# Optimization experiments

Measured on AMD Instinct MI355X. Metric: run time of the kernel, lower is better.

## Reference

```python
import jax, jax.numpy as jnp
import numpy as np

N = 100000      # n_nodes
D = 64          # d_model
E = 1_600_000   # n_edges
L = 3           # n_layers


def setup_inputs() -> dict:
    key = jax.random.key(0)
    ks = jax.random.split(key, 2 + 2 * L)
    x = jax.random.normal(ks[0], (N, D), dtype=jnp.float32)
    edge_index = jax.random.randint(ks[1], (2, E), 0, N, dtype=jnp.int32)
    inp = {"x": x, "edge_index": edge_index}
    scale = 1.0 / np.sqrt(D)
    for i in range(L):
        # GCNConv weight (glorot-ish init) and zero bias
        inp[f"W{i}"] = jax.random.uniform(ks[2 + 2 * i], (D, D), jnp.float32, -scale, scale)
        inp[f"b{i}"] = jnp.zeros((D,), jnp.float32)
    return inp


def gcn_conv(x, W, b, src, dst, num_nodes):
    # PyG GCNConv: h = x @ W, then D^{-1/2}(A+I)D^{-1/2} aggregation, then + b
    h = x @ W  # [N, D]
    ones = jnp.ones(dst.shape, dtype=h.dtype)
    deg = jax.ops.segment_sum(ones, dst, num_segments=num_nodes)  # [N]
    deg_inv_sqrt = jnp.where(deg > 0, jax.lax.rsqrt(jnp.maximum(deg, 1.0)), 0.0)
    norm = deg_inv_sqrt[src] * deg_inv_sqrt[dst]  # [E+N]
    msg = h[src] * norm[:, None]                  # gather + scale  [E+N, D]
    out = jax.ops.segment_sum(msg, dst, num_segments=num_nodes)  # scatter-add [N, D]
    return out + b


def reference(x, edge_index, W0, b0, W1, b1, W2, b2):
    num_nodes = x.shape[0]
    loop = jnp.arange(num_nodes, dtype=edge_index.dtype)
    src = jnp.concatenate([edge_index[0], loop])  # add self-loops
    dst = jnp.concatenate([edge_index[1], loop])
    h = x
    for W, b in ((W0, b0), (W1, b1), (W2, b2)):
        h = gcn_conv(h, W, b, src, dst, num_nodes)
        # F.dropout(training=self.training) is identity in eval mode
    return h
```

## Files before the change

kernel.cpp:

```cpp
#include <hip/hip_runtime.h>
#include <hip/hip_bf16.h>

#define D 64
#define RSHIFT 9
#define BNODES 512
#define MAXB 256
#define BCAP 10240
#define SCAP 14336
#define FH 72

typedef unsigned short ushort_t;
typedef unsigned int uint_t;
typedef short short8 __attribute__((ext_vector_type(8)));
typedef float floatx4 __attribute__((ext_vector_type(4)));

__device__ inline uint_t pk_bf16(float x, float y) {
    uint_t ux = __float_as_uint(x); ux = ux + 0x7fffu + ((ux >> 16) & 1u);
    uint_t uy = __float_as_uint(y); uy = uy + 0x7fffu + ((uy >> 16) & 1u);
    return (ux >> 16) | (uy & 0xffff0000u);
}
__device__ inline ushort_t rnd_bf16(float x) {
    uint_t u = __float_as_uint(x); u = u + 0x7fffu + ((u >> 16) & 1u);
    return (ushort_t)(u >> 16);
}

__global__ __launch_bounds__(256) void k_bucket(const int* __restrict__ src,
                                                const int* __restrict__ dst,
                                                int* __restrict__ bcur,
                                                int* __restrict__ ebuf,
                                                int E, int nb) {
    __shared__ int lcnt[MAXB];
    __shared__ int lbase[MAXB];
    int t = threadIdx.x;
    lcnt[t] = 0;
    __syncthreads();
    int base = blockIdx.x * 2048 + t * 8;
    int sv[8], dv[8], sl[8];
    if (base + 7 < E) {
        int4 a0 = *(const int4*)(src + base);
        int4 a1 = *(const int4*)(src + base + 4);
        int4 b0 = *(const int4*)(dst + base);
        int4 b1 = *(const int4*)(dst + base + 4);
        sv[0]=a0.x; sv[1]=a0.y; sv[2]=a0.z; sv[3]=a0.w;
        sv[4]=a1.x; sv[5]=a1.y; sv[6]=a1.z; sv[7]=a1.w;
        dv[0]=b0.x; dv[1]=b0.y; dv[2]=b0.z; dv[3]=b0.w;
        dv[4]=b1.x; dv[5]=b1.y; dv[6]=b1.z; dv[7]=b1.w;
    } else {
        #pragma unroll
        for (int j = 0; j < 8; ++j) {
            dv[j] = (base + j < E) ? dst[base + j] : -1;
            sv[j] = (base + j < E) ? src[base + j] : 0;
        }
    }
    #pragma unroll
    for (int j = 0; j < 8; ++j) {
        if (dv[j] >= 0) {
            int b = dv[j] >> RSHIFT;
            sl[j] = atomicAdd(&lcnt[b], 1);
        }
    }
    __syncthreads();
    if (t < nb) { int c = lcnt[t]; if (c) lbase[t] = atomicAdd(&bcur[t], c); }
    __syncthreads();
    #pragma unroll
    for (int j = 0; j < 8; ++j) {
        if (dv[j] >= 0) {
            int b = dv[j] >> RSHIFT;
            int slot = lbase[b] + sl[j];
            if (slot < BCAP)
                ebuf[(size_t)b * BCAP + slot] = (sv[j] << RSHIFT) | (dv[j] & (BNODES - 1));
        }
    }
}

__global__ __launch_bounds__(256) void k_csr(const int* __restrict__ ebuf,
                                             const int* __restrict__ bcur,
                                             int2* __restrict__ rowse,
                                             int* __restrict__ ssrc,
                                             float* __restrict__ dis,
                                             int N, int nb) {
    __shared__ int sseg[BCAP];
    __shared__ int lcnt[BNODES];
    __shared__ int lcur[BNODES];
    __shared__ int sums[256];
    int b = blockIdx.x;
    int t = threadIdx.x;
    int n = bcur[b];
    if (n > BCAP) n = BCAP;
    int node0 = b << RSHIFT;
    #pragma unroll
    for (int i = t; i < BNODES; i += 256) lcnt[i] = 0;
    __syncthreads();
    const int* seg = ebuf + (size_t)b * BCAP;
    for (int i = t * 4; i < n; i += 1024) {
        if (i + 3 < n) {
            int4 e = *(const int4*)(seg + i);
            *(int4*)(sseg + i) = e;
            atomicAdd(&lcnt[e.x & (BNODES - 1)], 1);
            atomicAdd(&lcnt[e.y & (BNODES - 1)], 1);
            atomicAdd(&lcnt[e.z & (BNODES - 1)], 1);
            atomicAdd(&lcnt[e.w & (BNODES - 1)], 1);
        } else {
            for (int j = 0; j < 4 && i + j < n; ++j) {
                int e = seg[i + j];
                sseg[i + j] = e;
                atomicAdd(&lcnt[e & (BNODES - 1)], 1);
            }
        }
    }
    __syncthreads();
    int idx = t * 2;
    int v0 = lcnt[idx], v1 = lcnt[idx + 1];
    int p0 = (v0 + 7) & ~7;
    int p1 = (v1 + 7) & ~7;
    int s = p0 + p1;
    sums[t] = s;
    __syncthreads();
    for (int off = 1; off < 256; off <<= 1) {
        int x = (t >= off) ? sums[t - off] : 0;
        __syncthreads();
        sums[t] += x;
        __syncthreads();
    }
    int run = sums[t] - s;
    int beg0 = b * SCAP + run;
    int beg1 = beg0 + p0;
    lcur[idx] = beg0;
    lcur[idx + 1] = beg1;
    int node = node0 + idx;
    if (node < N)     { rowse[node]     = make_int2(beg0, beg0 + p0); dis[node]     = rsqrtf((float)(v0 + 1)); }
    if (node + 1 < N) { rowse[node + 1] = make_int2(beg1, beg1 + p1); dis[node + 1] = rsqrtf((float)(v1 + 1)); }
    __syncthreads();
    for (int i = t * 4; i < n; i += 1024) {
        if (i + 3 < n) {
            int4 e = *(const int4*)(sseg + i);
            int q0 = atomicAdd(&lcur[e.x & (BNODES - 1)], 1); ssrc[q0] = e.x >> RSHIFT;
            int q1 = atomicAdd(&lcur[e.y & (BNODES - 1)], 1); ssrc[q1] = e.y >> RSHIFT;
            int q2 = atomicAdd(&lcur[e.z & (BNODES - 1)], 1); ssrc[q2] = e.z >> RSHIFT;
            int q3 = atomicAdd(&lcur[e.w & (BNODES - 1)], 1); ssrc[q3] = e.w >> RSHIFT;
        } else {
            for (int j = 0; j < 4 && i + j < n; ++j) {
                int e = sseg[i + j];
                int q = atomicAdd(&lcur[e & (BNODES - 1)], 1); ssrc[q] = e >> RSHIFT;
            }
        }
    }
    for (int k = v0; k < p0; ++k) ssrc[beg0 + k] = N;
    for (int k = v1; k < p1; ++k) ssrc[beg1 + k] = N;
}

__device__ __forceinline__ void stage_wt(const float* __restrict__ W,
                                         ushort_t* __restrict__ wt, int t) {
    const float4* W4 = (const float4*)W;
    for (int i = t; i < 1024; i += 256) {
        float4 w4 = W4[i];
        int k = i >> 4, n0 = (i & 15) * 4;
        wt[(n0 + 0) * FH + k] = rnd_bf16(w4.x);
        wt[(n0 + 1) * FH + k] = rnd_bf16(w4.y);
        wt[(n0 + 2) * FH + k] = rnd_bf16(w4.z);
        wt[(n0 + 3) * FH + k] = rnd_bf16(w4.w);
    }
}

__global__ __launch_bounds__(256) void k_gemm0(const float* __restrict__ x,
                                               const float* __restrict__ W,
                                               const float* __restrict__ dis,
                                               ushort_t* __restrict__ G, int N) {
    __shared__ ushort_t wt[64 * FH];
    int t = threadIdx.x;
    stage_wt(W, wt, t);
    __syncthreads();
    int wv = t >> 6, lane = t & 63;
    int m = lane & 15, quad = lane >> 4;
    int row = blockIdx.x * 64 + wv * 16 + m;
    long rowc = (row < N) ? row : (N - 1);
    float4 f0 = *(const float4*)(x + rowc * D + quad * 8);
    float4 f1 = *(const float4*)(x + rowc * D + quad * 8 + 4);
    float4 f2 = *(const float4*)(x + rowc * D + 32 + quad * 8);
    float4 f3 = *(const float4*)(x + rowc * D + 32 + quad * 8 + 4);
    union { short8 s; uint_t u[4]; } a0, a1;
    a0.u[0] = pk_bf16(f0.x, f0.y); a0.u[1] = pk_bf16(f0.z, f0.w);
    a0.u[2] = pk_bf16(f1.x, f1.y); a0.u[3] = pk_bf16(f1.z, f1.w);
    a1.u[0] = pk_bf16(f2.x, f2.y); a1.u[1] = pk_bf16(f2.z, f2.w);
    a1.u[2] = pk_bf16(f3.x, f3.y); a1.u[3] = pk_bf16(f3.z, f3.w);
    floatx4 acc[4];
    #pragma unroll
    for (int j = 0; j < 4; ++j) {
        short8 b0 = *(short8*)&wt[(j * 16 + m) * FH + quad * 8];
        short8 b1 = *(short8*)&wt[(j * 16 + m) * FH + 32 + quad * 8];
        floatx4 z = {0.f, 0.f, 0.f, 0.f};
        acc[j] = __builtin_amdgcn_mfma_f32_16x16x32_bf16(a0.s, b0, z, 0, 0, 0);
        acc[j] = __builtin_amdgcn_mfma_f32_16x16x32_bf16(a1.s, b1, acc[j], 0, 0, 0);
    }
    int rbase = blockIdx.x * 64 + wv * 16 + quad * 4;
    #pragma unroll
    for (int r = 0; r < 4; ++r) {
        int rr = rbase + r;
        if (rr < N) {
            float sc = dis[rr];
            #pragma unroll
            for (int j = 0; j < 4; ++j)
                G[(size_t)rr * D + j * 16 + m] = rnd_bf16(acc[j][r] * sc);
        }
    }
}

__device__ __forceinline__ void gather_node(const ushort_t* __restrict__ G,
                                            const int* __restrict__ ssrc,
                                            int beg, int end, int c8,
                                            int node, float a[8]) {
    #pragma unroll
    for (int j = 0; j < 8; ++j) a[j] = 0.f;
    #define ROW(i) (*(const uint4*)(G + (size_t)(i) * D + c8))
    #define ACC1(u)                                                        \
        {                                                                  \
            a[0] += __uint_as_float(u.x << 16);                            \
            a[1] += __uint_as_float(u.x & 0xffff0000u);                    \
            a[2] += __uint_as_float(u.y << 16);                            \
            a[3] += __uint_as_float(u.y & 0xffff0000u);                    \
            a[4] += __uint_as_float(u.z << 16);                            \
            a[5] += __uint_as_float(u.z & 0xffff0000u);                    \
            a[6] += __uint_as_float(u.w << 16);                            \
            a[7] += __uint_as_float(u.w & 0xffff0000u);                    \
        }
    uint4 su = ROW(node);
    int n8 = (end - beg) >> 3;
    const int4* sp = (const int4*)(ssrc + beg);
    if (n8 > 0) {
        int4 ia = sp[0], ib = sp[1];
        uint4 u0 = ROW(ia.x), u1 = ROW(ia.y), u2 = ROW(ia.z), u3 = ROW(ia.w);
        uint4 u4 = ROW(ib.x), u5 = ROW(ib.y), u6 = ROW(ib.z), u7 = ROW(ib.w);
        if (n8 > 1) { ia = sp[2]; ib = sp[3]; }
        for (int ch = 1; ch < n8; ++ch) {
            uint4 v0 = ROW(ia.x), v1 = ROW(ia.y), v2 = ROW(ia.z), v3 = ROW(ia.w);
            uint4 v4 = ROW(ib.x), v5 = ROW(ib.y), v6 = ROW(ib.z), v7 = ROW(ib.w);
            if (ch + 1 < n8) { ia = sp[2 * ch + 2]; ib = sp[2 * ch + 3]; }
            ACC1(u0); ACC1(u1); ACC1(u2); ACC1(u3);
            ACC1(u4); ACC1(u5); ACC1(u6); ACC1(u7);
            u0 = v0; u1 = v1; u2 = v2; u3 = v3;
            u4 = v4; u5 = v5; u6 = v6; u7 = v7;
        }
        ACC1(u0); ACC1(u1); ACC1(u2); ACC1(u3);
        ACC1(u4); ACC1(u5); ACC1(u6); ACC1(u7);
    }
    ACC1(su);
    #undef ACC1
    #undef ROW
}

__global__ __launch_bounds__(256) void k_fagg(const ushort_t* __restrict__ G,
                                              const float* __restrict__ dis,
                                              const int2* __restrict__ rowse,
                                              const int* __restrict__ ssrc,
                                              const float* __restrict__ bias,
                                              const float* __restrict__ W,
                                              ushort_t* __restrict__ Gout,
                                              int N) {
    __shared__ ushort_t hbuf[64 * FH];
    __shared__ ushort_t wt[64 * FH];
    int t = threadIdx.x;
    stage_wt(W, wt, t);
    int wv = t >> 6, lane = t & 63;
    int g = lane >> 3;
    int c8 = (lane & 7) * 8;
    int gbase = blockIdx.x * 64;
    float4 bv0 = *(const float4*)(bias + c8);
    float4 bv1 = *(const float4*)(bias + c8 + 4);
    for (int ii = 0; ii < 2; ++ii) {
        int idx = wv * 16 + ii * 8 + g;
        int node = gbase + idx;
        if (node < N) {
            int2 se = rowse[node];
            float di = dis[node];
            float a[8];
            gather_node(G, ssrc, se.x, se.y, c8, node, a);
            uint4 p;
            p.x = pk_bf16(a[0] * di + bv0.x, a[1] * di + bv0.y);
            p.y = pk_bf16(a[2] * di + bv0.z, a[3] * di + bv0.w);
            p.z = pk_bf16(a[4] * di + bv1.x, a[5] * di + bv1.y);
            p.w = pk_bf16(a[6] * di + bv1.z, a[7] * di + bv1.w);
            *(uint4*)&hbuf[idx * FH + c8] = p;
        }
    }
    __syncthreads();
    int m = lane & 15, quad = lane >> 4;
    short8 a0 = *(short8*)&hbuf[(wv * 16 + m) * FH + quad * 8];
    short8 a1 = *(short8*)&hbuf[(wv * 16 + m) * FH + 32 + quad * 8];
    floatx4 acc[4];
    #pragma unroll
    for (int j = 0; j < 4; ++j) {
        short8 b0 = *(short8*)&wt[(j * 16 + m) * FH + quad * 8];
        short8 b1 = *(short8*)&wt[(j * 16 + m) * FH + 32 + quad * 8];
        floatx4 z = {0.f, 0.f, 0.f, 0.f};
        acc[j] = __builtin_amdgcn_mfma_f32_16x16x32_bf16(a0, b0, z, 0, 0, 0);
        acc[j] = __builtin_amdgcn_mfma_f32_16x16x32_bf16(a1, b1, acc[j], 0, 0, 0);
    }
    int rbase = gbase + wv * 16 + quad * 4;
    #pragma unroll
    for (int r = 0; r < 4; ++r) {
        int row = rbase + r;
        if (row < N) {
            float sc = dis[row];
            #pragma unroll
            for (int j = 0; j < 4; ++j)
                Gout[(size_t)row * D + j * 16 + m] = rnd_bf16(acc[j][r] * sc);
        }
    }
}

__global__ __launch_bounds__(256) void k_agg(const ushort_t* __restrict__ G,
                                             const float* __restrict__ dis,
                                             const int2* __restrict__ rowse,
                                             const int* __restrict__ ssrc,
                                             const float* __restrict__ bias,
                                             float* __restrict__ out, int N) {
    int t = threadIdx.x;
    int wv = t >> 6, lane = t & 63;
    int g = lane >> 3;
    int c8 = (lane & 7) * 8;
    int node = blockIdx.x * 32 + wv * 8 + g;
    if (node >= N) return;
    int2 se = rowse[node];
    float di = dis[node];
    float a[8];
    gather_node(G, ssrc, se.x, se.y, c8, node, a);
    float4 bv0 = *(const float4*)(bias + c8);
    float4 bv1 = *(const float4*)(bias + c8 + 4);
    float4 r0, r1;
    r0.x = a[0] * di + bv0.x; r0.y = a[1] * di + bv0.y;
    r0.z = a[2] * di + bv0.z; r0.w = a[3] * di + bv0.w;
    r1.x = a[4] * di + bv1.x; r1.y = a[5] * di + bv1.y;
    r1.z = a[6] * di + bv1.z; r1.w = a[7] * di + bv1.w;
    float4* op = (float4*)(out + (size_t)node * D + c8);
    op[0] = r0;
    op[1] = r1;
}


extern "C" void kernel_launch(void* const* d_in, const int* in_sizes, int n_in,
                              void* d_out, int out_size, void* d_ws, size_t ws_size,
                              hipStream_t stream) {
    const float* x  = (const float*)d_in[0];
    const int*   ei = (const int*)d_in[1];
    const float* W0 = (const float*)d_in[2];
    const float* b0 = (const float*)d_in[3];
    const float* W1 = (const float*)d_in[4];
    const float* b1 = (const float*)d_in[5];
    const float* W2 = (const float*)d_in[6];
    const float* b2 = (const float*)d_in[7];
    float* out = (float*)d_out;

    const int N = in_sizes[0] / D;
    const int E = in_sizes[1] / 2;
    const int* e_src = ei;
    const int* e_dst = ei + E;

    const int nb = (N + BNODES - 1) >> RSHIFT;

    size_t rowsz   = (size_t)(N + 1) * D;
    ushort_t* B0   = (ushort_t*)d_ws;
    ushort_t* B1   = B0 + rowsz;
    float* dis     = (float*)(B1 + rowsz);
    int2*  rowse   = (int2*)(dis + N);
    int*   ssrc    = (int*)(rowse + N);
    int*   bcur    = ssrc + (size_t)nb * SCAP;
    int*   ebuf    = (int*)d_ws;

    const int gG64 = (N + 63) / 64;
    const int gAgg = (N + 31) / 32;

    hipMemsetAsync(bcur, 0, MAXB * sizeof(int), stream);
    hipMemsetAsync(B0 + (size_t)N * D, 0, D * sizeof(ushort_t), stream);
    hipMemsetAsync(B1 + (size_t)N * D, 0, D * sizeof(ushort_t), stream);

    k_bucket<<<(E + 2047) / 2048, 256, 0, stream>>>(e_src, e_dst, bcur, ebuf, E, nb);
    k_csr<<<nb, 256, 0, stream>>>(ebuf, bcur, rowse, ssrc, dis, N, nb);

    k_gemm0<<<gG64, 256, 0, stream>>>(x, W0, dis, B0, N);
    k_fagg<<<gG64, 256, 0, stream>>>(B0, dis, rowse, ssrc, b0, W1, B1, N);
    k_fagg<<<gG64, 256, 0, stream>>>(B1, dis, rowse, ssrc, b1, W2, B0, N);
    k_agg<<<gAgg, 256, 0, stream>>>(B0, dis, rowse, ssrc, b2, out, N);
}
```

Baseline: 240.4 us.

## Replace two-pass bucketed CSR build with degree count, scan, and global-atomic scatter

Swaps the bucket-then-local-sort CSR construction for three kernels. The first counts in-degree with global atomics, the second does a per-block padded scan that writes row ranges and cursors, and the third scatters source indices using a global atomic cursor per destination. This drops the intermediate edge bucket buffer and the shared-memory sort pass. In exchange it adds many contended global atomics on random addresses and an extra kernel launch, and the scatter writes land in nondeterministic order within each row.

```diff
diff --git a/kernel.cpp b/kernel.cpp
--- a/kernel.cpp
+++ b/kernel.cpp
@@ -4,8 +4,6 @@
 #define D 64
 #define RSHIFT 9
 #define BNODES 512
-#define MAXB 256
-#define BCAP 10240
 #define SCAP 14336
 #define FH 72
 
@@ -24,93 +22,35 @@
     return (ushort_t)(u >> 16);
 }
 
-__global__ __launch_bounds__(256) void k_bucket(const int* __restrict__ src,
-                                                const int* __restrict__ dst,
-                                                int* __restrict__ bcur,
-                                                int* __restrict__ ebuf,
-                                                int E, int nb) {
-    __shared__ int lcnt[MAXB];
-    __shared__ int lbase[MAXB];
-    int t = threadIdx.x;
-    lcnt[t] = 0;
-    __syncthreads();
-    int base = blockIdx.x * 2048 + t * 8;
-    int sv[8], dv[8], sl[8];
+__global__ __launch_bounds__(256) void k_deg(const int* __restrict__ dst,
+                                             int* __restrict__ deg, int E) {
+    int base = blockIdx.x * 2048 + threadIdx.x * 8;
     if (base + 7 < E) {
-        int4 a0 = *(const int4*)(src + base);
-        int4 a1 = *(const int4*)(src + base + 4);
         int4 b0 = *(const int4*)(dst + base);
         int4 b1 = *(const int4*)(dst + base + 4);
-        sv[0]=a0.x; sv[1]=a0.y; sv[2]=a0.z; sv[3]=a0.w;
-        sv[4]=a1.x; sv[5]=a1.y; sv[6]=a1.z; sv[7]=a1.w;
-        dv[0]=b0.x; dv[1]=b0.y; dv[2]=b0.z; dv[3]=b0.w;
-        dv[4]=b1.x; dv[5]=b1.y; dv[6]=b1.z; dv[7]=b1.w;
+        atomicAdd(&deg[b0.x], 1); atomicAdd(&deg[b0.y], 1);
+        atomicAdd(&deg[b0.z], 1); atomicAdd(&deg[b0.w], 1);
+        atomicAdd(&deg[b1.x], 1); atomicAdd(&deg[b1.y], 1);
+        atomicAdd(&deg[b1.z], 1); atomicAdd(&deg[b1.w], 1);
     } else {
-        #pragma unroll
-        for (int j = 0; j < 8; ++j) {
-            dv[j] = (base + j < E) ? dst[base + j] : -1;
-            sv[j] = (base + j < E) ? src[base + j] : 0;
-        }
-    }
-    #pragma unroll
-    for (int j = 0; j < 8; ++j) {
-        if (dv[j] >= 0) {
-            int b = dv[j] >> RSHIFT;
-            sl[j] = atomicAdd(&lcnt[b], 1);
-        }
-    }
-    __syncthreads();
-    if (t < nb) { int c = lcnt[t]; if (c) lbase[t] = atomicAdd(&bcur[t], c); }
-    __syncthreads();
-    #pragma unroll
-    for (int j = 0; j < 8; ++j) {
-        if (dv[j] >= 0) {
-            int b = dv[j] >> RSHIFT;
-            int slot = lbase[b] + sl[j];
-            if (slot < BCAP)
-                ebuf[(size_t)b * BCAP + slot] = (sv[j] << RSHIFT) | (dv[j] & (BNODES - 1));
-        }
-    }
-}
-
-__global__ __launch_bounds__(256) void k_csr(const int* __restrict__ ebuf,
-                                             const int* __restrict__ bcur,
-                                             int2* __restrict__ rowse,
-                                             int* __restrict__ ssrc,
-                                             float* __restrict__ dis,
-                                             int N, int nb) {
-    __shared__ int sseg[BCAP];
-    __shared__ int lcnt[BNODES];
-    __shared__ int lcur[BNODES];
+        for (int j = 0; j < 8 && base + j < E; ++j)
+            atomicAdd(&deg[dst[base + j]], 1);
+    }
+}
+
+__global__ __launch_bounds__(256) void k_scan(const int* __restrict__ deg,
+                                              int2* __restrict__ rowse,
+                                              int* __restrict__ cur,
+                                              int* __restrict__ ssrc,
+                                              float* __restrict__ dis,
+                                              int N) {
     __shared__ int sums[256];
     int b = blockIdx.x;
     int t = threadIdx.x;
-    int n = bcur[b];
-    if (n > BCAP) n = BCAP;
-    int node0 = b << RSHIFT;
-    #pragma unroll
-    for (int i = t; i < BNODES; i += 256) lcnt[i] = 0;
-    __syncthreads();
-    const int* seg = ebuf + (size_t)b * BCAP;
-    for (int i = t * 4; i < n; i += 1024) {
-        if (i + 3 < n) {
-            int4 e = *(const int4*)(seg + i);
-            *(int4*)(sseg + i) = e;
-            atomicAdd(&lcnt[e.x & (BNODES - 1)], 1);
-            atomicAdd(&lcnt[e.y & (BNODES - 1)], 1);
-            atomicAdd(&lcnt[e.z & (BNODES - 1)], 1);
-            atomicAdd(&lcnt[e.w & (BNODES - 1)], 1);
-        } else {
-            for (int j = 0; j < 4 && i + j < n; ++j) {
-                int e = seg[i + j];
-                sseg[i + j] = e;
-                atomicAdd(&lcnt[e & (BNODES - 1)], 1);
-            }
-        }
-    }
-    __syncthreads();
     int idx = t * 2;
-    int v0 = lcnt[idx], v1 = lcnt[idx + 1];
+    int node = (b << RSHIFT) + idx;
+    int v0 = (node < N) ? deg[node] : 0;
+    int v1 = (node + 1 < N) ? deg[node + 1] : 0;
     int p0 = (v0 + 7) & ~7;
     int p1 = (v1 + 7) & ~7;
     int s = p0 + p1;
@@ -125,28 +65,46 @@
     int run = sums[t] - s;
     int beg0 = b * SCAP + run;
     int beg1 = beg0 + p0;
-    lcur[idx] = beg0;
-    lcur[idx + 1] = beg1;
-    int node = node0 + idx;
-    if (node < N)     { rowse[node]     = make_int2(beg0, beg0 + p0); dis[node]     = rsqrtf((float)(v0 + 1)); }
-    if (node + 1 < N) { rowse[node + 1] = make_int2(beg1, beg1 + p1); dis[node + 1] = rsqrtf((float)(v1 + 1)); }
-    __syncthreads();
-    for (int i = t * 4; i < n; i += 1024) {
-        if (i + 3 < n) {
-            int4 e = *(const int4*)(sseg + i);
-            int q0 = atomicAdd(&lcur[e.x & (BNODES - 1)], 1); ssrc[q0] = e.x >> RSHIFT;
-            int q1 = atomicAdd(&lcur[e.y & (BNODES - 1)], 1); ssrc[q1] = e.y >> RSHIFT;
-            int q2 = atomicAdd(&lcur[e.z & (BNODES - 1)], 1); ssrc[q2] = e.z >> RSHIFT;
-            int q3 = atomicAdd(&lcur[e.w & (BNODES - 1)], 1); ssrc[q3] = e.w >> RSHIFT;
-        } else {
-            for (int j = 0; j < 4 && i + j < n; ++j) {
-                int e = sseg[i + j];
-                int q = atomicAdd(&lcur[e & (BNODES - 1)], 1); ssrc[q] = e >> RSHIFT;
-            }
-        }
-    }
-    for (int k = v0; k < p0; ++k) ssrc[beg0 + k] = N;
-    for (int k = v1; k < p1; ++k) ssrc[beg1 + k] = N;
+    if (node < N) {
+        rowse[node] = make_int2(beg0, beg0 + p0);
+        dis[node] = rsqrtf((float)(v0 + 1));
+        cur[node] = beg0;
+        for (int k = v0; k < p0; ++k) ssrc[beg0 + k] = N;
+    }
+    if (node + 1 < N) {
+        rowse[node + 1] = make_int2(beg1, beg1 + p1);
+        dis[node + 1] = rsqrtf((float)(v1 + 1));
+        cur[node + 1] = beg1;
+        for (int k = v1; k < p1; ++k) ssrc[beg1 + k] = N;
+    }
+}
+
+__global__ __launch_bounds__(256) void k_scatter(const int* __restrict__ src,
+                                                 const int* __restrict__ dst,
+                                                 int* __restrict__ cur,
+                                                 int* __restrict__ ssrc, int E) {
+    int base = blockIdx.x * 2048 + threadIdx.x * 8;
+    int sv[8], dv[8];
+    if (base + 7 < E) {
+        int4 a0 = *(const int4*)(src + base);
+        int4 a1 = *(const int4*)(src + base + 4);
+        int4 b0 = *(const int4*)(dst + base);
+        int4 b1 = *(const int4*)(dst + base + 4);
+        sv[0]=a0.x; sv[1]=a0.y; sv[2]=a0.z; sv[3]=a0.w;
+        sv[4]=a1.x; sv[5]=a1.y; sv[6]=a1.z; sv[7]=a1.w;
+        dv[0]=b0.x; dv[1]=b0.y; dv[2]=b0.z; dv[3]=b0.w;
+        dv[4]=b1.x; dv[5]=b1.y; dv[6]=b1.z; dv[7]=b1.w;
+        int q[8];
+        #pragma unroll
+        for (int j = 0; j < 8; ++j) q[j] = atomicAdd(&cur[dv[j]], 1);
+        #pragma unroll
+        for (int j = 0; j < 8; ++j) ssrc[q[j]] = sv[j];
+    } else {
+        for (int j = 0; j < 8 && base + j < E; ++j) {
+            int q = atomicAdd(&cur[dst[base + j]], 1);
+            ssrc[q] = src[base + j];
+        }
+    }
 }
 
 __device__ __forceinline__ void stage_wt(const float* __restrict__ W,
@@ -363,18 +321,20 @@
     float* dis     = (float*)(B1 + rowsz);
     int2*  rowse   = (int2*)(dis + N);
     int*   ssrc    = (int*)(rowse + N);
-    int*   bcur    = ssrc + (size_t)nb * SCAP;
-    int*   ebuf    = (int*)d_ws;
-
+    int*   deg     = ssrc + (size_t)nb * SCAP;
+    int*   cur     = deg + N;
+
+    const int gE   = (E + 2047) / 2048;
     const int gG64 = (N + 63) / 64;
     const int gAgg = (N + 31) / 32;
 
-    hipMemsetAsync(bcur, 0, MAXB * sizeof(int), stream);
+    hipMemsetAsync(deg, 0, (size_t)N * sizeof(int), stream);
     hipMemsetAsync(B0 + (size_t)N * D, 0, D * sizeof(ushort_t), stream);
     hipMemsetAsync(B1 + (size_t)N * D, 0, D * sizeof(ushort_t), stream);
 
-    k_bucket<<<(E + 2047) / 2048, 256, 0, stream>>>(e_src, e_dst, bcur, ebuf, E, nb);
-    k_csr<<<nb, 256, 0, stream>>>(ebuf, bcur, rowse, ssrc, dis, N, nb);
+    k_deg<<<gE, 256, 0, stream>>>(e_dst, deg, E);
+    k_scan<<<nb, 256, 0, stream>>>(deg, rowse, cur, ssrc, dis, N);
+    k_scatter<<<gE, 256, 0, stream>>>(e_src, e_dst, cur, ssrc, E);
 
     k_gemm0<<<gG64, 256, 0, stream>>>(x, W0, dis, B0, N);
     k_fagg<<<gG64, 256, 0, stream>>>(B0, dis, rowse, ssrc, b0, W1, B1, N);
```

Result: slower. 393.5 us (+63.7%).

## Sort nodes by degree class within each bucket to balance gather work

Applied to the files above, without the earlier changes.

k_csr now builds a per-bucket node permutation that groups nodes by their 8-edge chunk count, using a small shared-memory histogram and scan. The aggregation kernels k_fagg and k_agg read node ids through this permutation, so nodes sharing a wave have similar neighbor-loop trip counts. The aim is to cut lane divergence and idle time in the gather loops. The cost is an extra indirection load per node, scattered output-row writes, zero-filling padded rows in the MFMA staging buffer, and a little extra work in k_csr.

```diff
diff --git a/kernel.cpp b/kernel.cpp
--- a/kernel.cpp
+++ b/kernel.cpp
@@ -78,11 +78,13 @@
                                              int2* __restrict__ rowse,
                                              int* __restrict__ ssrc,
                                              float* __restrict__ dis,
+                                             int* __restrict__ nperm,
                                              int N, int nb) {
     __shared__ int sseg[BCAP];
     __shared__ int lcnt[BNODES];
     __shared__ int lcur[BNODES];
     __shared__ int sums[256];
+    __shared__ int chist[33];
     int b = blockIdx.x;
     int t = threadIdx.x;
     int n = bcur[b];
@@ -147,6 +149,27 @@
     }
     for (int k = v0; k < p0; ++k) ssrc[beg0 + k] = N;
     for (int k = v1; k < p1; ++k) ssrc[beg1 + k] = N;
+    __syncthreads();
+    if (t < 33) chist[t] = 0;
+    __syncthreads();
+    int cnt = N - node0; if (cnt > BNODES) cnt = BNODES; if (cnt < 0) cnt = 0;
+    for (int i = t; i < cnt; i += 256) {
+        int c = (lcnt[i] + 7) >> 3; if (c > 32) c = 32;
+        atomicAdd(&chist[c], 1);
+    }
+    __syncthreads();
+    if (t == 0) {
+        int acc = 0;
+        for (int c = 0; c <= 32; ++c) { int v = chist[c]; chist[c] = acc; acc += v; }
+    }
+    __syncthreads();
+    for (int i = t; i < cnt; i += 256) {
+        int c = (lcnt[i] + 7) >> 3; if (c > 32) c = 32;
+        int r = atomicAdd(&chist[c], 1);
+        nperm[(b << RSHIFT) + r] = node0 + i;
+    }
+    for (int i = t; i < BNODES; i += 256)
+        if (i >= cnt) nperm[(b << RSHIFT) + i] = N;
 }
 
 __device__ __forceinline__ void stage_wt(const float* __restrict__ W,
@@ -252,6 +275,7 @@
                                               const float* __restrict__ dis,
                                               const int2* __restrict__ rowse,
                                               const int* __restrict__ ssrc,
+                                              const int* __restrict__ nperm,
                                               const float* __restrict__ bias,
                                               const float* __restrict__ W,
                                               ushort_t* __restrict__ Gout,
@@ -268,7 +292,7 @@
     float4 bv1 = *(const float4*)(bias + c8 + 4);
     for (int ii = 0; ii < 2; ++ii) {
         int idx = wv * 16 + ii * 8 + g;
-        int node = gbase + idx;
+        int node = nperm[gbase + idx];
         if (node < N) {
             int2 se = rowse[node];
             float di = dis[node];
@@ -280,6 +304,9 @@
             p.z = pk_bf16(a[4] * di + bv1.x, a[5] * di + bv1.y);
             p.w = pk_bf16(a[6] * di + bv1.z, a[7] * di + bv1.w);
             *(uint4*)&hbuf[idx * FH + c8] = p;
+        } else {
+            uint4 z = {0u, 0u, 0u, 0u};
+            *(uint4*)&hbuf[idx * FH + c8] = z;
         }
     }
     __syncthreads();
@@ -295,15 +322,17 @@
         acc[j] = __builtin_amdgcn_mfma_f32_16x16x32_bf16(a0, b0, z, 0, 0, 0);
         acc[j] = __builtin_amdgcn_mfma_f32_16x16x32_bf16(a1, b1, acc[j], 0, 0, 0);
     }
-    int rbase = gbase + wv * 16 + quad * 4;
+    int sbase = wv * 16 + quad * 4;
+    int4 nd4 = *(const int4*)&nperm[gbase + sbase];
+    int nds[4] = {nd4.x, nd4.y, nd4.z, nd4.w};
     #pragma unroll
     for (int r = 0; r < 4; ++r) {
-        int row = rbase + r;
-        if (row < N) {
-            float sc = dis[row];
+        int nodeR = nds[r];
+        if (nodeR < N) {
+            float sc = dis[nodeR];
             #pragma unroll
             for (int j = 0; j < 4; ++j)
-                Gout[(size_t)row * D + j * 16 + m] = rnd_bf16(acc[j][r] * sc);
+                Gout[(size_t)nodeR * D + j * 16 + m] = rnd_bf16(acc[j][r] * sc);
         }
     }
 }
@@ -312,13 +341,15 @@
                                              const float* __restrict__ dis,
                                              const int2* __restrict__ rowse,
                                              const int* __restrict__ ssrc,
+                                             const int* __restrict__ nperm,
                                              const float* __restrict__ bias,
                                              float* __restrict__ out, int N) {
     int t = threadIdx.x;
     int wv = t >> 6, lane = t & 63;
     int g = lane >> 3;
     int c8 = (lane & 7) * 8;
-    int node = blockIdx.x * 32 + wv * 8 + g;
+    int slot = blockIdx.x * 32 + wv * 8 + g;
+    int node = nperm[slot];
     if (node >= N) return;
     int2 se = rowse[node];
     float di = dis[node];
@@ -364,20 +395,21 @@
     int2*  rowse   = (int2*)(dis + N);
     int*   ssrc    = (int*)(rowse + N);
     int*   bcur    = ssrc + (size_t)nb * SCAP;
+    int*   nperm   = bcur + MAXB;
     int*   ebuf    = (int*)d_ws;
 
     const int gG64 = (N + 63) / 64;
-    const int gAgg = (N + 31) / 32;
+    const int gAgg = nb * 16;
 
     hipMemsetAsync(bcur, 0, MAXB * sizeof(int), stream);
     hipMemsetAsync(B0 + (size_t)N * D, 0, D * sizeof(ushort_t), stream);
     hipMemsetAsync(B1 + (size_t)N * D, 0, D * sizeof(ushort_t), stream);
 
     k_bucket<<<(E + 2047) / 2048, 256, 0, stream>>>(e_src, e_dst, bcur, ebuf, E, nb);
-    k_csr<<<nb, 256, 0, stream>>>(ebuf, bcur, rowse, ssrc, dis, N, nb);
+    k_csr<<<nb, 256, 0, stream>>>(ebuf, bcur, rowse, ssrc, dis, nperm, N, nb);
 
     k_gemm0<<<gG64, 256, 0, stream>>>(x, W0, dis, B0, N);
-    k_fagg<<<gG64, 256, 0, stream>>>(B0, dis, rowse, ssrc, b0, W1, B1, N);
-    k_fagg<<<gG64, 256, 0, stream>>>(B1, dis, rowse, ssrc, b1, W2, B0, N);
-    k_agg<<<gAgg, 256, 0, stream>>>(B0, dis, rowse, ssrc, b2, out, N);
-}
+    k_fagg<<<gG64, 256, 0, stream>>>(B0, dis, rowse, ssrc, nperm, b0, W1, B1, N);
+    k_fagg<<<gG64, 256, 0, stream>>>(B1, dis, rowse, ssrc, nperm, b1, W2, B0, N);
+    k_agg<<<gAgg, 256, 0, stream>>>(B0, dis, rowse, ssrc, nperm, b2, out, N);
+}
```

After: 254.0 us. +5.6%, slower.
